# Kernel tuning notes

Hardware: AMD Instinct MI355X
Metric: run time of the kernel (lower is better)

## Reference

```python
import jax, jax.numpy as jnp
import numpy as np

B, IC, HC = 262144, 128, 128


def setup_inputs() -> dict:
    key = jax.random.key(0)
    ks = jax.random.split(key, 12)
    s_ih = 1.0 / np.sqrt(IC)
    s_hh = 1.0 / np.sqrt(HC)
    return {
        "x": jax.random.normal(ks[0], (B, IC), jnp.float32),
        "u": jax.random.uniform(ks[1], (B, 1), jnp.float32),
        "h": jax.random.normal(ks[2], (B, HC), jnp.float32) * 0.1,
        "c": jax.random.normal(ks[3], (B, HC), jnp.float32) * 0.1,
        "delta_u": jax.random.uniform(ks[4], (B, 1), jnp.float32),
        "skip": jax.random.randint(ks[5], (B,), 0, 2) == 1,
        # LSTMCell params (PyTorch gate order: i, f, g, o)
        "W_ih": jax.random.normal(ks[6], (4 * HC, IC), jnp.float32) * s_ih,
        "W_hh": jax.random.normal(ks[7], (4 * HC, HC), jnp.float32) * s_hh,
        "b_ih": jnp.zeros((4 * HC,), jnp.float32),
        "b_hh": jnp.zeros((4 * HC,), jnp.float32),
        # Linear(hc -> 1), bias initialized to 1 per the module
        "lin_w": jax.random.normal(ks[8], (1, HC), jnp.float32) * s_hh,
        "lin_b": jnp.ones((1,), jnp.float32),
    }


def _ste_round(u):
    # straight-through estimator: forward round, identity backward
    return u + jax.lax.stop_gradient(jnp.round(u) - u)


def reference(x, u, h, c, delta_u, skip, W_ih, W_hh, b_ih, b_hh, lin_w, lin_b):
    bu = _ste_round(u)  # [B,1]

    # --- no-skip branch: LSTM cell + update-gate linear ---
    gates = x @ W_ih.T + b_ih + h @ W_hh.T + b_hh  # [B,4*HC]
    i, f, g, o = jnp.split(gates, 4, axis=1)
    i = jax.nn.sigmoid(i)
    f = jax.nn.sigmoid(f)
    g = jnp.tanh(g)
    o = jax.nn.sigmoid(o)
    nc = f * c + i * g
    nh = o * jnp.tanh(nc)
    new_h_n = nh * bu
    new_c_n = nc * bu
    delta_u_n = jax.nn.sigmoid(new_c_n @ lin_w.T + lin_b)  # [B,1]
    new_u_n = delta_u_n * bu

    # --- skip branch: decay state, accumulate u ---
    keep = 1.0 - bu
    new_h_s = h * keep
    new_c_s = c * keep
    new_u_s = jnp.clip(u + delta_u, 0.0, 1.0) * keep

    # --- recombine by skip mask (equivalent to the gather/scatter routing) ---
    sk = skip[:, None]
    new_u = jnp.where(sk, new_u_s, new_u_n)
    new_h = jnp.where(sk, new_h_s, new_h_n)
    new_c = jnp.where(sk, new_c_s, new_c_n)
    d_u = jnp.where(sk, delta_u, delta_u_n)

    n_skips_after = jnp.ceil(0.5 / new_u) - 1.0
    return new_u, (new_h, new_c), d_u, n_skips_after
```

## Files before the change

kernel.cpp:

```cpp
#include <hip/hip_runtime.h>


typedef _Float16 half8  __attribute__((ext_vector_type(8)));
typedef _Float16 half4v __attribute__((ext_vector_type(4)));
typedef float    float4v __attribute__((ext_vector_type(4)));

#define B_ROWS 262144
#define TM 64
#define TG 32
#define XPITCH_H 136
#define XPLANE_H (TG * XPITCH_H)
#define WCOMP  131072

__device__ __forceinline__ float sigmoidf_(float v) { return 1.0f / (1.0f + __expf(-v)); }
__device__ __forceinline__ float tanhf_(float v) {
    float ax = fabsf(v);
    float t = __expf(-2.0f * ax);
    float r = (1.0f - t) / (1.0f + t);
    return copysignf(r, v);
}

__global__ void prep_kernel(const float* __restrict__ W_ih, const float* __restrict__ W_hh,
                            const float* __restrict__ b_ih, const float* __restrict__ b_hh,
                            _Float16* __restrict__ Wp, float* __restrict__ bias,
                            int* __restrict__ counter) {
    if (blockIdx.x == 0 && threadIdx.x == 0) *counter = 0;
    int idx = blockIdx.x * 256 + threadIdx.x;
    int n = idx >> 8, k = idx & 255;
    float v = (k < 128) ? W_ih[n * 128 + k] : W_hh[n * 128 + (k - 128)];
    _Float16 wh = (_Float16)v;
    _Float16 wl = (_Float16)(v - (float)wh);
    int kb = k >> 5, quad = (k >> 3) & 3, j = k & 7;
    int nt = n >> 4, n16 = n & 15, lane = quad * 16 + n16;
    int base = (kb * 32 + nt) * 512 + lane * 8 + j;
    Wp[base] = wh;
    Wp[WCOMP + base] = wl;
    if (idx < 512) bias[idx] = b_ih[idx] + b_hh[idx];
}

__global__ void classify_kernel(const float* __restrict__ u, const float* __restrict__ h,
                                const float* __restrict__ c, const float* __restrict__ delta_u,
                                const int* __restrict__ skip, const float* __restrict__ lin_b,
                                int* __restrict__ counter, int* __restrict__ act_idx,
                                float* __restrict__ out) {
    __shared__ int s_cat[TM];
    const int tid = threadIdx.x;
    const int m0  = blockIdx.x * TM;

    float* out_u  = out;
    float* out_h  = out + (size_t)B_ROWS;
    float* out_c  = out + (size_t)B_ROWS * 129;
    float* out_du = out + (size_t)B_ROWS * 257;
    float* out_ns = out + (size_t)B_ROWS * 258;

    if (tid < TM) {
        int row = m0 + tid;
        float uv  = u[row];
        float duv = delta_u[row];
        int   sk  = skip[row];
        float buv = rintf(uv);
        bool active = (sk == 0) && (buv != 0.0f);
        s_cat[tid] = active ? 2 : ((sk != 0 && buv == 0.0f) ? 1 : 0);

        if (!active) {
            float nu, duo;
            if (sk != 0) {
                nu  = (buv == 0.0f) ? fminf(fmaxf(uv + duv, 0.0f), 1.0f) : 0.0f;
                duo = duv;
            } else {
                nu  = 0.0f;
                duo = sigmoidf_(lin_b[0]);
            }
            float nsk = ceilf(0.5f / nu) - 1.0f;
            if (!__builtin_isfinite(nsk)) nsk = 1.0e30f;
            out_u[row]  = nu;
            out_du[row] = duo;
            out_ns[row] = nsk;
        }
        unsigned long long mask = __ballot(active);
        int nact = __popcll(mask);
        int base = 0;
        if (tid == 0 && nact) base = atomicAdd(counter, nact);
        base = __shfl(base, 0, 64);
        if (active) {
            int pos = __popcll(mask & ((1ull << tid) - 1ull));
            act_idx[base + pos] = row;
        }
    }
    __syncthreads();

    #pragma unroll
    for (int it = 0; it < 8; ++it) {
        int r = it * 8 + (tid >> 5);
        int cat = s_cat[r];
        if (cat == 2) continue;
        size_t m = (size_t)(m0 + r);
        int c4 = (tid & 31) * 4;
        float4v vh = {0.f, 0.f, 0.f, 0.f}, vc = {0.f, 0.f, 0.f, 0.f};
        if (cat == 1) {
            vh = *(const float4v*)&h[m * 128 + c4];
            vc = *(const float4v*)&c[m * 128 + c4];
        }
        *(float4v*)&out_h[m * 128 + c4] = vh;
        *(float4v*)&out_c[m * 128 + c4] = vc;
    }
}

__launch_bounds__(256, 4)
__global__ void gemm_kernel(const float* __restrict__ x, const float* __restrict__ h,
                            const float* __restrict__ c,
                            const float* __restrict__ lin_w, const float* __restrict__ lin_b,
                            const _Float16* __restrict__ Wp, const float* __restrict__ bias,
                            const int* __restrict__ counter, const int* __restrict__ act_idx,
                            float* __restrict__ out) {
    const int n_act = *counter;
    if ((int)blockIdx.x * TG >= n_act) return;

    __shared__ __align__(16) _Float16 Xs[2 * XPLANE_H];
    __shared__ float zw[4][TG];
    __shared__ int   s_rid[TG];

    const int tid = threadIdx.x;

    if (tid < TG) {
        int g = blockIdx.x * TG + tid;
        s_rid[tid] = act_idx[g < n_act ? g : n_act - 1];
    }
    __syncthreads();

    const int lane = tid & 63, w = tid >> 6;
    const int n16 = lane & 15, quad = lane >> 4;

    int ntid[8];
    #pragma unroll
    for (int g = 0; g < 4; ++g)
        #pragma unroll
        for (int p = 0; p < 2; ++p) ntid[g * 2 + p] = w * 2 + g * 8 + p;

    float4v acc[8][2];
    #pragma unroll
    for (int t = 0; t < 8; ++t)
        #pragma unroll
        for (int mt = 0; mt < 2; ++mt) acc[t][mt] = (float4v){0.f, 0.f, 0.f, 0.f};

    #pragma unroll 1
    for (int kh = 0; kh < 2; ++kh) {
        #pragma unroll
        for (int i = 0; i < 4; ++i) {
            int idx = i * 256 + tid;
            int r = idx >> 5, c4 = (idx & 31) * 4;
            size_t srow = (size_t)s_rid[r];
            float4v v;
            if (kh == 0) v = *(const float4v*)&x[srow * 128 + c4];
            else         v = *(const float4v*)&h[srow * 128 + c4];
            half4v hi, lo;
            #pragma unroll
            for (int e = 0; e < 4; ++e) {
                _Float16 hh = (_Float16)v[e];
                hi[e] = hh;
                lo[e] = (_Float16)(v[e] - (float)hh);
            }
            *(half4v*)&Xs[r * XPITCH_H + c4]             = hi;
            *(half4v*)&Xs[XPLANE_H + r * XPITCH_H + c4]  = lo;
        }
        __syncthreads();

        #pragma unroll
        for (int kbl = 0; kbl < 4; ++kbl) {
            const int kbg = kh * 4 + kbl;
            half8 ah[2], al[2];
            const int koff = kbl * 32 + quad * 8;
            #pragma unroll
            for (int mt = 0; mt < 2; ++mt) {
                int m = mt * 16 + n16;
                ah[mt] = *(const half8*)&Xs[m * XPITCH_H + koff];
                al[mt] = *(const half8*)&Xs[XPLANE_H + m * XPITCH_H + koff];
            }
            #pragma unroll
            for (int t = 0; t < 8; ++t) {
                const _Float16* bp = Wp + (size_t)(kbg * 32 + ntid[t]) * 512 + lane * 8;
                half8 bh = *(const half8*)bp;
                half8 bl = *(const half8*)(bp + WCOMP);
                #pragma unroll
                for (int mt = 0; mt < 2; ++mt) {
                    acc[t][mt] = __builtin_amdgcn_mfma_f32_16x16x32_f16(ah[mt], bh, acc[t][mt], 0, 0, 0);
                    acc[t][mt] = __builtin_amdgcn_mfma_f32_16x16x32_f16(al[mt], bh, acc[t][mt], 0, 0, 0);
                    acc[t][mt] = __builtin_amdgcn_mfma_f32_16x16x32_f16(ah[mt], bl, acc[t][mt], 0, 0, 0);
                }
            }
        }
        __syncthreads();
    }

    float* out_u  = out;
    float* out_h  = out + (size_t)B_ROWS;
    float* out_c  = out + (size_t)B_ROWS * 129;
    float* out_du = out + (size_t)B_ROWS * 257;
    float* out_ns = out + (size_t)B_ROWS * 258;

    float zpart[2][4];
    #pragma unroll
    for (int mt = 0; mt < 2; ++mt)
        #pragma unroll
        for (int reg = 0; reg < 4; ++reg) zpart[mt][reg] = 0.f;

    #pragma unroll
    for (int p = 0; p < 2; ++p) {
        int hc = w * 32 + p * 16 + n16;
        float bi = bias[hc], bf = bias[hc + 128], bg = bias[hc + 256], bo = bias[hc + 384];
        float lw = lin_w[hc];
        #pragma unroll
        for (int mt = 0; mt < 2; ++mt) {
            #pragma unroll
            for (int reg = 0; reg < 4; ++reg) {
                int row = mt * 16 + quad * 4 + reg;
                bool valid = blockIdx.x * TG + row < n_act;
                size_t m = (size_t)s_rid[row];
                float iv = sigmoidf_(acc[0 * 2 + p][mt][reg] + bi);
                float fv = sigmoidf_(acc[1 * 2 + p][mt][reg] + bf);
                float gv = tanhf_  (acc[2 * 2 + p][mt][reg] + bg);
                float ov = sigmoidf_(acc[3 * 2 + p][mt][reg] + bo);
                float cin = c[m * 128 + hc];
                float ncv = fv * cin + iv * gv;
                float nhv = ov * tanhf_(ncv);
                if (valid) {
                    out_h[m * 128 + hc] = nhv;
                    out_c[m * 128 + hc] = ncv;
                }
                zpart[mt][reg] += ncv * lw;
            }
        }
    }

    #pragma unroll
    for (int mt = 0; mt < 2; ++mt)
        #pragma unroll
        for (int reg = 0; reg < 4; ++reg) {
            float v = zpart[mt][reg];
            v += __shfl_xor(v, 1, 64);
            v += __shfl_xor(v, 2, 64);
            v += __shfl_xor(v, 4, 64);
            v += __shfl_xor(v, 8, 64);
            if (n16 == 0) zw[w][mt * 16 + quad * 4 + reg] = v;
        }
    __syncthreads();

    if (tid < TG) {
        int row = tid;
        if (blockIdx.x * TG + row < n_act) {
            float z = zw[0][row] + zw[1][row] + zw[2][row] + zw[3][row];
            float dun = sigmoidf_(z + lin_b[0]);
            float nsk = ceilf(0.5f / dun) - 1.0f;
            if (!__builtin_isfinite(nsk)) nsk = 1.0e30f;
            size_t m = (size_t)s_rid[row];
            out_u[m]  = dun;
            out_du[m] = dun;
            out_ns[m] = nsk;
        }
    }
}

extern "C" void kernel_launch(void* const* d_in, const int* in_sizes, int n_in,
                              void* d_out, int out_size, void* d_ws, size_t ws_size,
                              hipStream_t stream) {
    const float* x     = (const float*)d_in[0];
    const float* u     = (const float*)d_in[1];
    const float* h     = (const float*)d_in[2];
    const float* c     = (const float*)d_in[3];
    const float* du    = (const float*)d_in[4];
    const int*   skip  = (const int*)d_in[5];
    const float* W_ih  = (const float*)d_in[6];
    const float* W_hh  = (const float*)d_in[7];
    const float* b_ih  = (const float*)d_in[8];
    const float* b_hh  = (const float*)d_in[9];
    const float* lin_w = (const float*)d_in[10];
    const float* lin_b = (const float*)d_in[11];
    float* outp = (float*)d_out;

    _Float16* Wp   = (_Float16*)d_ws;
    float* bias    = (float*)((char*)d_ws + 2 * WCOMP * sizeof(_Float16));
    int* counter   = (int*)((char*)d_ws + 2 * WCOMP * sizeof(_Float16) + 2048);
    int* act_idx   = (int*)((char*)d_ws + 2 * WCOMP * sizeof(_Float16) + 2048 + 64);

    prep_kernel<<<512, 256, 0, stream>>>(W_ih, W_hh, b_ih, b_hh, Wp, bias, counter);
    classify_kernel<<<B_ROWS / TM, 256, 0, stream>>>(u, h, c, du, skip, lin_b,
                                                     counter, act_idx, outp);
    gemm_kernel<<<B_ROWS / TG, 256, 0, stream>>>(x, h, c, lin_w, lin_b, Wp, bias,
                                                 counter, act_idx, outp);
}
```

Before: 697.0 us.

## Stage full K tile in LDS once and batch weight loads per k-block

Loads both the x and h halves of each gathered row tile into LDS in a single pass, doubling the shared-memory pitch, so the kernel needs only one barrier phase instead of two. The k-loop now issues all 16 global weight fragment loads for a k-block up front before the MFMAs, giving more memory-level parallelism. The price is doubled LDS per block and more live registers, so launch bounds drop from 4 to 3 blocks per CU, which lowers occupancy.

```diff
diff --git a/kernel.cpp b/kernel.cpp
--- a/kernel.cpp
+++ b/kernel.cpp
@@ -8,8 +8,8 @@
 #define B_ROWS 262144
 #define TM 64
 #define TG 32
-#define XPITCH_H 136
-#define XPLANE_H (TG * XPITCH_H)
+#define XPITCH 264
+#define XPLANE (TG * XPITCH)
 #define WCOMP  131072
 
 __device__ __forceinline__ float sigmoidf_(float v) { return 1.0f / (1.0f + __expf(-v)); }
@@ -106,7 +106,7 @@
     }
 }
 
-__launch_bounds__(256, 4)
+__launch_bounds__(256, 3)
 __global__ void gemm_kernel(const float* __restrict__ x, const float* __restrict__ h,
                             const float* __restrict__ c,
                             const float* __restrict__ lin_w, const float* __restrict__ lin_b,
@@ -116,7 +116,7 @@
     const int n_act = *counter;
     if ((int)blockIdx.x * TG >= n_act) return;
 
-    __shared__ __align__(16) _Float16 Xs[2 * XPLANE_H];
+    __shared__ __align__(16) _Float16 Xs[2 * XPLANE];
     __shared__ float zw[4][TG];
     __shared__ int   s_rid[TG];
 
@@ -128,6 +128,26 @@
     }
     __syncthreads();
 
+    #pragma unroll
+    for (int i = 0; i < 8; ++i) {
+        int idx = i * 256 + tid;
+        int r = idx >> 6, c4 = (idx & 63) * 4;
+        size_t srow = (size_t)s_rid[r];
+        float4v v;
+        if (c4 < 128) v = *(const float4v*)&x[srow * 128 + c4];
+        else          v = *(const float4v*)&h[srow * 128 + (c4 - 128)];
+        half4v hi, lo;
+        #pragma unroll
+        for (int e = 0; e < 4; ++e) {
+            _Float16 hh = (_Float16)v[e];
+            hi[e] = hh;
+            lo[e] = (_Float16)(v[e] - (float)hh);
+        }
+        *(half4v*)&Xs[r * XPITCH + c4]          = hi;
+        *(half4v*)&Xs[XPLANE + r * XPITCH + c4] = lo;
+    }
+    __syncthreads();
+
     const int lane = tid & 63, w = tid >> 6;
     const int n16 = lane & 15, quad = lane >> 4;
 
@@ -144,52 +164,30 @@
         for (int mt = 0; mt < 2; ++mt) acc[t][mt] = (float4v){0.f, 0.f, 0.f, 0.f};
 
     #pragma unroll 1
-    for (int kh = 0; kh < 2; ++kh) {
-        #pragma unroll
-        for (int i = 0; i < 4; ++i) {
-            int idx = i * 256 + tid;
-            int r = idx >> 5, c4 = (idx & 31) * 4;
-            size_t srow = (size_t)s_rid[r];
-            float4v v;
-            if (kh == 0) v = *(const float4v*)&x[srow * 128 + c4];
-            else         v = *(const float4v*)&h[srow * 128 + c4];
-            half4v hi, lo;
-            #pragma unroll
-            for (int e = 0; e < 4; ++e) {
-                _Float16 hh = (_Float16)v[e];
-                hi[e] = hh;
-                lo[e] = (_Float16)(v[e] - (float)hh);
-            }
-            *(half4v*)&Xs[r * XPITCH_H + c4]             = hi;
-            *(half4v*)&Xs[XPLANE_H + r * XPITCH_H + c4]  = lo;
-        }
-        __syncthreads();
-
-        #pragma unroll
-        for (int kbl = 0; kbl < 4; ++kbl) {
-            const int kbg = kh * 4 + kbl;
-            half8 ah[2], al[2];
-            const int koff = kbl * 32 + quad * 8;
+    for (int kb = 0; kb < 8; ++kb) {
+        half8 bh[8], bl[8];
+        #pragma unroll
+        for (int t = 0; t < 8; ++t) {
+            const _Float16* bp = Wp + (size_t)(kb * 32 + ntid[t]) * 512 + lane * 8;
+            bh[t] = *(const half8*)bp;
+            bl[t] = *(const half8*)(bp + WCOMP);
+        }
+        half8 ah[2], al[2];
+        const int koff = kb * 32 + quad * 8;
+        #pragma unroll
+        for (int mt = 0; mt < 2; ++mt) {
+            int m = mt * 16 + n16;
+            ah[mt] = *(const half8*)&Xs[m * XPITCH + koff];
+            al[mt] = *(const half8*)&Xs[XPLANE + m * XPITCH + koff];
+        }
+        #pragma unroll
+        for (int t = 0; t < 8; ++t)
             #pragma unroll
             for (int mt = 0; mt < 2; ++mt) {
-                int m = mt * 16 + n16;
-                ah[mt] = *(const half8*)&Xs[m * XPITCH_H + koff];
-                al[mt] = *(const half8*)&Xs[XPLANE_H + m * XPITCH_H + koff];
+                acc[t][mt] = __builtin_amdgcn_mfma_f32_16x16x32_f16(ah[mt], bh[t], acc[t][mt], 0, 0, 0);
+                acc[t][mt] = __builtin_amdgcn_mfma_f32_16x16x32_f16(al[mt], bh[t], acc[t][mt], 0, 0, 0);
+                acc[t][mt] = __builtin_amdgcn_mfma_f32_16x16x32_f16(ah[mt], bl[t], acc[t][mt], 0, 0, 0);
             }
-            #pragma unroll
-            for (int t = 0; t < 8; ++t) {
-                const _Float16* bp = Wp + (size_t)(kbg * 32 + ntid[t]) * 512 + lane * 8;
-                half8 bh = *(const half8*)bp;
-                half8 bl = *(const half8*)(bp + WCOMP);
-                #pragma unroll
-                for (int mt = 0; mt < 2; ++mt) {
-                    acc[t][mt] = __builtin_amdgcn_mfma_f32_16x16x32_f16(ah[mt], bh, acc[t][mt], 0, 0, 0);
-                    acc[t][mt] = __builtin_amdgcn_mfma_f32_16x16x32_f16(al[mt], bh, acc[t][mt], 0, 0, 0);
-                    acc[t][mt] = __builtin_amdgcn_mfma_f32_16x16x32_f16(ah[mt], bl, acc[t][mt], 0, 0, 0);
-                }
-            }
-        }
-        __syncthreads();
     }
 
     float* out_u  = out;
```

After: 605.2 us. 1.15x faster.
